# Performance work log

Measured on AMD Instinct MI355X. Metric: run time of the kernel, lower is better.

## Reference

```python
import jax, jax.numpy as jnp
import numpy as np

N_NODES = 100000
N_EDGES = 3200000
EMB_DIM = 128


def setup_inputs() -> dict:
    key = jax.random.key(0)
    k_emb, k_w1, k_w2, k_e = jax.random.split(key, 4)
    emb = jax.random.normal(k_emb, (N_NODES, EMB_DIM), dtype=jnp.float32)
    W1 = jax.random.normal(k_w1, (EMB_DIM, 64), dtype=jnp.float32) * (1.0 / np.sqrt(EMB_DIM))
    b1 = jnp.zeros((64,), dtype=jnp.float32)
    W2 = jax.random.normal(k_w2, (64, 32), dtype=jnp.float32) * (1.0 / np.sqrt(64))
    b2 = jnp.zeros((32,), dtype=jnp.float32)
    edge_index = jax.random.randint(k_e, (2, N_EDGES), 0, N_NODES, dtype=jnp.int64)
    return {"embedding": emb, "W1": W1, "b1": b1, "W2": W2, "b2": b2,
            "edge_index": edge_index}


def gcn_conv(x, W, b, src, dst, n):
    # PyG GCNConv defaults: add self-loops, symmetric normalization D^-1/2 (A+I) D^-1/2,
    # linear transform first, then gather-scale-scatter aggregation, then bias.
    xw = x @ W                                                  # [N, out]
    ones = jnp.ones(src.shape, dtype=xw.dtype)
    deg = jax.ops.segment_sum(ones, dst, num_segments=n) + 1.0  # in-degree + self-loop
    dis = jax.lax.rsqrt(deg)                                    # deg >= 1 always
    norm = dis[src] * dis[dst]                                  # [E]
    agg = jax.ops.segment_sum(xw[src] * norm[:, None], dst, num_segments=n)
    agg = agg + (dis * dis)[:, None] * xw                       # self-loop messages
    return agg + b


def reference(embedding, W1, b1, W2, b2, edge_index):
    n = embedding.shape[0]
    src, dst = edge_index[0], edge_index[1]
    # encode
    h = jax.nn.relu(gcn_conv(embedding, W1, b1, src, dst, n))
    z = gcn_conv(h, W2, b2, src, dst, n)                        # [N, 32]
    # decode: per-edge gather-dot-sigmoid
    logits = jnp.sum(z[src] * z[dst], axis=1)                   # [E]
    return jax.nn.sigmoid(logits)
```

## Files before the change

### kernel.cpp

```cpp
#include <hip/hip_runtime.h>
#include <hip/hip_bf16.h>
#include <math.h>

#define NN 100000
#define NE 3200000
#define NPAD 100096
#define NB 196
#define BN 512
#define EPB 8192
#define NBLK 391

typedef __attribute__((ext_vector_type(8))) short short8;
typedef __attribute__((ext_vector_type(4))) float floatx4;

__device__ __forceinline__ unsigned short bf16_of(float x) {
    __hip_bfloat16 h = __float2bfloat16(x);
    return *(unsigned short*)&h;
}
__device__ __forceinline__ unsigned pack2(float a, float b) {
    return (unsigned)bf16_of(a) | ((unsigned)bf16_of(b) << 16);
}
__device__ __forceinline__ float lo_f(unsigned u) { return __uint_as_float(u << 16); }
__device__ __forceinline__ float hi_f(unsigned u) { return __uint_as_float(u & 0xffff0000u); }
__device__ __forceinline__ void acc8(float* a, uint4 r) {
    a[0] += lo_f(r.x); a[1] += hi_f(r.x);
    a[2] += lo_f(r.y); a[3] += hi_f(r.y);
    a[4] += lo_f(r.z); a[5] += hi_f(r.z);
    a[6] += lo_f(r.w); a[7] += hi_f(r.w);
}

__global__ __launch_bounds__(256) void hist_kernel(const int* __restrict__ dst,
                                                   int* __restrict__ blkhist) {
    __shared__ int cnt[NB];
    int t = threadIdx.x;
    for (int i = t; i < NB; i += 256) cnt[i] = 0;
    __syncthreads();
    int e0 = blockIdx.x * EPB;
    int e1 = min(e0 + EPB, NE);
    for (int e = e0 + t; e < e1; e += 256) atomicAdd(&cnt[dst[e] >> 9], 1);
    __syncthreads();
    for (int i = t; i < NB; i += 256) blkhist[i * NBLK + blockIdx.x] = cnt[i];
}

__global__ __launch_bounds__(64) void scanA_kernel(int* __restrict__ blkhist,
                                                   int* __restrict__ totals) {
    int j = blockIdx.x, lane = threadIdx.x;
    int base = j * NBLK;
    int carry = 0;
    for (int c = 0; c < NBLK; c += 64) {
        int b = c + lane;
        int v = (b < NBLK) ? blkhist[base + b] : 0;
        int inc = v;
#pragma unroll
        for (int m = 1; m < 64; m <<= 1) {
            int u = __shfl_up(inc, m, 64);
            if (lane >= m) inc += u;
        }
        if (b < NBLK) blkhist[base + b] = carry + inc - v;
        carry += __shfl(inc, 63, 64);
    }
    if (lane == 0) totals[j] = carry;
}

__global__ __launch_bounds__(256) void scanB_kernel(const int* __restrict__ totals,
                                                    int* __restrict__ bucket_base) {
    __shared__ int sm[NB];
    int t = threadIdx.x;
    if (t < NB) sm[t] = totals[t];
    __syncthreads();
    if (t == 0) {
        int r = 0;
        for (int i = 0; i < NB; ++i) { bucket_base[i] = r; r += sm[i]; }
        bucket_base[NB] = r;
    }
}

__global__ __launch_bounds__(256) void scatter_kernel(const int* __restrict__ src,
                                                      const int* __restrict__ dst,
                                                      const int* __restrict__ blkhist,
                                                      const int* __restrict__ bucket_base,
                                                      int* __restrict__ staged) {
    __shared__ int cnt[NB];
    __shared__ int lbase[NB + 1];
    __shared__ int gbase[NB];
    __shared__ int sbuf[EPB];
    __shared__ unsigned char sbkt[EPB];
    int t = threadIdx.x;
    for (int i = t; i < NB; i += 256) cnt[i] = 0;
    __syncthreads();
    int e0 = blockIdx.x * EPB;
    int e1 = min(e0 + EPB, NE);
    int cn = e1 - e0;
    for (int e = e0 + t; e < e1; e += 256) atomicAdd(&cnt[dst[e] >> 9], 1);
    __syncthreads();
    if (t < 64) {
        int v[4]; int s = 0;
#pragma unroll
        for (int k = 0; k < 4; ++k) { int idx = t * 4 + k; v[k] = (idx < NB) ? cnt[idx] : 0; s += v[k]; }
        int inc = s;
#pragma unroll
        for (int m = 1; m < 64; m <<= 1) {
            int u = __shfl_up(inc, m, 64);
            if (t >= m) inc += u;
        }
        int run = inc - s;
#pragma unroll
        for (int k = 0; k < 4; ++k) { int idx = t * 4 + k; if (idx < NB) lbase[idx] = run; run += v[k]; }
        if (t == 63) lbase[NB] = inc;
    }
    __syncthreads();
    for (int i = t; i < NB; i += 256) {
        gbase[i] = bucket_base[i] + blkhist[i * NBLK + blockIdx.x];
        cnt[i] = lbase[i];
    }
    __syncthreads();
    for (int e = e0 + t; e < e1; e += 256) {
        int s = src[e], d = dst[e];
        int bk = d >> 9;
        int r = atomicAdd(&cnt[bk], 1);
        sbuf[r] = (s << 9) | (d & (BN - 1));
        sbkt[r] = (unsigned char)bk;
    }
    __syncthreads();
    for (int i = t; i < cn; i += 256) {
        int bk = sbkt[i];
        staged[gbase[bk] + i - lbase[bk]] = sbuf[i];
    }
}

__global__ __launch_bounds__(256) void fine_kernel(const int* __restrict__ staged,
                                                   const int* __restrict__ bucket_base,
                                                   int* __restrict__ offset,
                                                   float* __restrict__ dis,
                                                   int* __restrict__ csr_src) {
    __shared__ int hist[BN];
    __shared__ int offs[BN];
    __shared__ int cur[BN];
    int t = threadIdx.x, j = blockIdx.x;
    int bb = bucket_base[j], be = bucket_base[j + 1];
    for (int i = t; i < BN; i += 256) hist[i] = 0;
    __syncthreads();
    for (int e = bb + t; e < be; e += 256) atomicAdd(&hist[staged[e] & (BN - 1)], 1);
    __syncthreads();
    if (t < 64) {
        int v[8]; int s = 0;
#pragma unroll
        for (int k = 0; k < 8; ++k) { v[k] = hist[t * 8 + k]; s += v[k]; }
        int inc = s;
#pragma unroll
        for (int m = 1; m < 64; m <<= 1) {
            int u = __shfl_up(inc, m, 64);
            if (t >= m) inc += u;
        }
        int run = inc - s;
#pragma unroll
        for (int k = 0; k < 8; ++k) { offs[t * 8 + k] = run; run += v[k]; }
    }
    __syncthreads();
    for (int l = t; l < BN; l += 256) {
        cur[l] = offs[l];
        int n = j * BN + l;
        if (n < NN) {
            offset[n] = bb + offs[l];
            dis[n] = rsqrtf((float)hist[l] + 1.0f);
        }
    }
    if (j == NB - 1 && t == 0) offset[NN] = NE;
    __syncthreads();
    for (int e = bb + t; e < be; e += 256) {
        int p = staged[e];
        int r = atomicAdd(&cur[p & (BN - 1)], 1);
        csr_src[bb + r] = p >> 9;
    }
}

__global__ __launch_bounds__(256) void mm1_kernel(const float* __restrict__ x,
                                                  const float* __restrict__ W,
                                                  const float* __restrict__ dis,
                                                  unsigned short* __restrict__ y) {
    __shared__ unsigned short Wt[64][136];
    int t = threadIdx.x;
    for (int i = t; i < 128 * 64; i += 256) {
        int k = i >> 6, n = i & 63;
        Wt[n][k] = bf16_of(W[i]);
    }
    __syncthreads();
    int wave = t >> 6, lane = t & 63;
    int quad = lane >> 4, n16 = lane & 15;
    short8 bfr[4][4];
#pragma unroll
    for (int s = 0; s < 4; ++s)
#pragma unroll
        for (int tt = 0; tt < 4; ++tt)
            bfr[s][tt] = *(const short8*)&Wt[tt * 16 + n16][s * 32 + quad * 8];
    int tile0 = (blockIdx.x * 4 + wave) * 4;
#pragma unroll 1
    for (int it = 0; it < 4; ++it) {
        int tile = tile0 + it;
        if (tile >= 6250) break;
        int m0 = tile * 16;
        const float* xp = x + (size_t)(m0 + n16) * 128 + quad * 8;
        floatx4 acc0 = {0,0,0,0}, acc1 = {0,0,0,0}, acc2 = {0,0,0,0}, acc3 = {0,0,0,0};
#pragma unroll
        for (int s = 0; s < 4; ++s) {
            float4 lo = *(const float4*)(xp + s * 32);
            float4 hi = *(const float4*)(xp + s * 32 + 4);
            short8 a;
            a[0] = (short)bf16_of(lo.x); a[1] = (short)bf16_of(lo.y);
            a[2] = (short)bf16_of(lo.z); a[3] = (short)bf16_of(lo.w);
            a[4] = (short)bf16_of(hi.x); a[5] = (short)bf16_of(hi.y);
            a[6] = (short)bf16_of(hi.z); a[7] = (short)bf16_of(hi.w);
            acc0 = __builtin_amdgcn_mfma_f32_16x16x32_bf16(a, bfr[s][0], acc0, 0, 0, 0);
            acc1 = __builtin_amdgcn_mfma_f32_16x16x32_bf16(a, bfr[s][1], acc1, 0, 0, 0);
            acc2 = __builtin_amdgcn_mfma_f32_16x16x32_bf16(a, bfr[s][2], acc2, 0, 0, 0);
            acc3 = __builtin_amdgcn_mfma_f32_16x16x32_bf16(a, bfr[s][3], acc3, 0, 0, 0);
        }
#pragma unroll
        for (int r = 0; r < 4; ++r) {
            int ro = m0 + quad * 4 + r;
            float sc = dis[ro];
            unsigned short* yp = y + (size_t)ro * 64 + n16;
            yp[0]  = bf16_of(acc0[r] * sc);
            yp[16] = bf16_of(acc1[r] * sc);
            yp[32] = bf16_of(acc2[r] * sc);
            yp[48] = bf16_of(acc3[r] * sc);
        }
    }
}

__global__ __launch_bounds__(256) void mm2_kernel(const unsigned short* __restrict__ h,
                                                  const float* __restrict__ W,
                                                  const float* __restrict__ dis,
                                                  unsigned short* __restrict__ y) {
    __shared__ unsigned short Wt[32][72];
    int t = threadIdx.x;
    for (int i = t; i < 64 * 32; i += 256) {
        int k = i >> 5, n = i & 31;
        Wt[n][k] = bf16_of(W[i]);
    }
    __syncthreads();
    int wave = t >> 6, lane = t & 63;
    int quad = lane >> 4, n16 = lane & 15;
    short8 bfr[2][2];
#pragma unroll
    for (int s = 0; s < 2; ++s)
#pragma unroll
        for (int tt = 0; tt < 2; ++tt)
            bfr[s][tt] = *(const short8*)&Wt[tt * 16 + n16][s * 32 + quad * 8];
    int tile0 = (blockIdx.x * 4 + wave) * 4;
#pragma unroll 1
    for (int it = 0; it < 4; ++it) {
        int tile = tile0 + it;
        if (tile >= 6250) break;
        int m0 = tile * 16;
        const unsigned short* hp = h + (size_t)(m0 + n16) * 64 + quad * 8;
        floatx4 acc0 = {0,0,0,0}, acc1 = {0,0,0,0};
#pragma unroll
        for (int s = 0; s < 2; ++s) {
            short8 a = *(const short8*)(hp + s * 32);
            acc0 = __builtin_amdgcn_mfma_f32_16x16x32_bf16(a, bfr[s][0], acc0, 0, 0, 0);
            acc1 = __builtin_amdgcn_mfma_f32_16x16x32_bf16(a, bfr[s][1], acc1, 0, 0, 0);
        }
#pragma unroll
        for (int r = 0; r < 4; ++r) {
            int ro = m0 + quad * 4 + r;
            float sc = dis[ro];
            unsigned short* yp = y + (size_t)ro * 32 + n16;
            yp[0]  = bf16_of(acc0[r] * sc);
            yp[16] = bf16_of(acc1[r] * sc);
        }
    }
}

__global__ __launch_bounds__(256) void agg64_kernel(const uint4* __restrict__ ys4,
                                                    const float* __restrict__ dis,
                                                    const int* __restrict__ offset,
                                                    const int* __restrict__ csr_src,
                                                    const float* __restrict__ b,
                                                    uint4* __restrict__ h4) {
    int tid = blockIdx.x * 256 + threadIdx.x;
    int nd = tid >> 3, c = tid & 7;
    if (nd >= NN) return;
    int start = offset[nd], end = offset[nd + 1];
    float acc[8] = {0, 0, 0, 0, 0, 0, 0, 0};
    acc8(acc, ys4[(size_t)nd * 8 + c]);
    int i = start;
    int n8 = start + ((end - start) & ~7);
    for (; i < n8; i += 8) {
        int s0 = csr_src[i],     s1 = csr_src[i + 1], s2 = csr_src[i + 2], s3 = csr_src[i + 3];
        int s4 = csr_src[i + 4], s5 = csr_src[i + 5], s6 = csr_src[i + 6], s7 = csr_src[i + 7];
        uint4 r0 = ys4[(size_t)s0 * 8 + c];
        uint4 r1 = ys4[(size_t)s1 * 8 + c];
        uint4 r2 = ys4[(size_t)s2 * 8 + c];
        uint4 r3 = ys4[(size_t)s3 * 8 + c];
        uint4 r4 = ys4[(size_t)s4 * 8 + c];
        uint4 r5 = ys4[(size_t)s5 * 8 + c];
        uint4 r6 = ys4[(size_t)s6 * 8 + c];
        uint4 r7 = ys4[(size_t)s7 * 8 + c];
        acc8(acc, r0); acc8(acc, r1); acc8(acc, r2); acc8(acc, r3);
        acc8(acc, r4); acc8(acc, r5); acc8(acc, r6); acc8(acc, r7);
    }
    for (; i < end; ++i) acc8(acc, ys4[(size_t)csr_src[i] * 8 + c]);
    float ds = dis[nd];
    const float4 bv0 = *(const float4*)&b[c * 8];
    const float4 bv1 = *(const float4*)&b[c * 8 + 4];
    uint4 o;
    o.x = pack2(fmaxf(fmaf(ds, acc[0], bv0.x), 0.f), fmaxf(fmaf(ds, acc[1], bv0.y), 0.f));
    o.y = pack2(fmaxf(fmaf(ds, acc[2], bv0.z), 0.f), fmaxf(fmaf(ds, acc[3], bv0.w), 0.f));
    o.z = pack2(fmaxf(fmaf(ds, acc[4], bv1.x), 0.f), fmaxf(fmaf(ds, acc[5], bv1.y), 0.f));
    o.w = pack2(fmaxf(fmaf(ds, acc[6], bv1.z), 0.f), fmaxf(fmaf(ds, acc[7], bv1.w), 0.f));
    h4[(size_t)nd * 8 + c] = o;
}

__global__ __launch_bounds__(256) void agg32_kernel(const uint4* __restrict__ ys4,
                                                    const float* __restrict__ dis,
                                                    const int* __restrict__ offset,
                                                    const int* __restrict__ csr_src,
                                                    const float* __restrict__ b,
                                                    uint4* __restrict__ z4) {
    int tid = blockIdx.x * 256 + threadIdx.x;
    int nd = tid >> 2, c = tid & 3;
    if (nd >= NN) return;
    int start = offset[nd], end = offset[nd + 1];
    float acc[8] = {0, 0, 0, 0, 0, 0, 0, 0};
    acc8(acc, ys4[(size_t)nd * 4 + c]);
    int i = start;
    int n8 = start + ((end - start) & ~7);
    for (; i < n8; i += 8) {
        int s0 = csr_src[i],     s1 = csr_src[i + 1], s2 = csr_src[i + 2], s3 = csr_src[i + 3];
        int s4 = csr_src[i + 4], s5 = csr_src[i + 5], s6 = csr_src[i + 6], s7 = csr_src[i + 7];
        uint4 r0 = ys4[(size_t)s0 * 4 + c];
        uint4 r1 = ys4[(size_t)s1 * 4 + c];
        uint4 r2 = ys4[(size_t)s2 * 4 + c];
        uint4 r3 = ys4[(size_t)s3 * 4 + c];
        uint4 r4 = ys4[(size_t)s4 * 4 + c];
        uint4 r5 = ys4[(size_t)s5 * 4 + c];
        uint4 r6 = ys4[(size_t)s6 * 4 + c];
        uint4 r7 = ys4[(size_t)s7 * 4 + c];
        acc8(acc, r0); acc8(acc, r1); acc8(acc, r2); acc8(acc, r3);
        acc8(acc, r4); acc8(acc, r5); acc8(acc, r6); acc8(acc, r7);
    }
    for (; i < end; ++i) acc8(acc, ys4[(size_t)csr_src[i] * 4 + c]);
    float ds = dis[nd];
    const float4 bv0 = *(const float4*)&b[c * 8];
    const float4 bv1 = *(const float4*)&b[c * 8 + 4];
    uint4 o;
    o.x = pack2(fmaf(ds, acc[0], bv0.x), fmaf(ds, acc[1], bv0.y));
    o.y = pack2(fmaf(ds, acc[2], bv0.z), fmaf(ds, acc[3], bv0.w));
    o.z = pack2(fmaf(ds, acc[4], bv1.x), fmaf(ds, acc[5], bv1.y));
    o.w = pack2(fmaf(ds, acc[6], bv1.z), fmaf(ds, acc[7], bv1.w));
    z4[(size_t)nd * 4 + c] = o;
}

__global__ __launch_bounds__(256) void decode_kernel(const uint4* __restrict__ z4,
                                                     const int* __restrict__ src,
                                                     const int* __restrict__ dst,
                                                     float* __restrict__ out) {
    int tid = blockIdx.x * 256 + threadIdx.x;
    int e = tid >> 2, k = tid & 3;
    if (e >= NE) return;
    int s = src[e], d = dst[e];
    uint4 ra = z4[(size_t)s * 4 + k];
    uint4 rb = z4[(size_t)d * 4 + k];
    float acc;
    acc  = lo_f(ra.x) * lo_f(rb.x) + hi_f(ra.x) * hi_f(rb.x);
    acc += lo_f(ra.y) * lo_f(rb.y) + hi_f(ra.y) * hi_f(rb.y);
    acc += lo_f(ra.z) * lo_f(rb.z) + hi_f(ra.z) * hi_f(rb.z);
    acc += lo_f(ra.w) * lo_f(rb.w) + hi_f(ra.w) * hi_f(rb.w);
#pragma unroll
    for (int m = 2; m >= 1; m >>= 1) acc += __shfl_xor(acc, m, 4);
    if (k == 0) out[e] = 1.0f / (1.0f + expf(-acc));
}

extern "C" void kernel_launch(void* const* d_in, const int* in_sizes, int n_in,
                              void* d_out, int out_size, void* d_ws, size_t ws_size,
                              hipStream_t stream) {
    const float* emb = (const float*)d_in[0];
    const float* W1  = (const float*)d_in[1];
    const float* b1  = (const float*)d_in[2];
    const float* W2  = (const float*)d_in[3];
    const float* b2  = (const float*)d_in[4];
    const int*   ei  = (const int*)d_in[5];
    const int* src = ei;
    const int* dst = ei + NE;
    float* out = (float*)d_out;

    char* w = (char*)d_ws;
    int*   offset      = (int*)w;           w += (size_t)NPAD * 4;
    float* dis         = (float*)w;         w += (size_t)NPAD * 4;
    int*   bucket_base = (int*)w;           w += 1024;
    int*   totals      = (int*)w;           w += 1024;
    int*   blkhist     = (int*)w;           w += 307200;
    int*   csr_src     = (int*)w;           w += (size_t)NE * 4;
    int*   staged      = (int*)w;           w += (size_t)NE * 4;
    unsigned short* ysbuf = (unsigned short*)w; w += (size_t)NN * 64 * 2;
    unsigned short* h  = (unsigned short*)w;
    unsigned short* ys1 = ysbuf;
    unsigned short* ys2 = ysbuf;
    unsigned short* z   = ysbuf + (size_t)NN * 32;

    hist_kernel<<<NBLK, 256, 0, stream>>>(dst, blkhist);
    scanA_kernel<<<NB, 64, 0, stream>>>(blkhist, totals);
    scanB_kernel<<<1, 256, 0, stream>>>(totals, bucket_base);
    scatter_kernel<<<NBLK, 256, 0, stream>>>(src, dst, blkhist, bucket_base, staged);
    fine_kernel<<<NB, 256, 0, stream>>>(staged, bucket_base, offset, dis, csr_src);

    mm1_kernel<<<391, 256, 0, stream>>>(emb, W1, dis, ys1);
    agg64_kernel<<<(NN * 8) / 256, 256, 0, stream>>>((const uint4*)ys1, dis, offset, csr_src, b1, (uint4*)h);

    mm2_kernel<<<391, 256, 0, stream>>>(h, W2, dis, ys2);
    agg32_kernel<<<(NN * 4 + 255) / 256, 256, 0, stream>>>((const uint4*)ys2, dis, offset, csr_src, b2, (uint4*)z);

    decode_kernel<<<(NE * 4) / 256, 256, 0, stream>>>((const uint4*)z, src, dst, out);
}
```

Baseline: 363.3 us.

## Fuse layer-1 aggregation with second matmul and use fp16 dot2 in decode

The layer-1 aggregation now keeps each 32-node tile of ReLU'd hidden rows in shared memory and runs the 64x32 MFMA matmul in the same kernel. This removes the global write and re-read of the hidden matrix and one kernel launch. Separately, z is stored as fp16 instead of bf16 so the decode kernel can use the packed fdot2 instruction for the per-edge dot product. The scatter bucket-tag array widens to 16-bit, and workspace buffers are laid out separately. Costs: only half the waves do the fused matmul, the block has an extra barrier, and fp16 has narrower range than bf16.

```diff
diff --git a/kernel.cpp b/kernel.cpp
--- a/kernel.cpp
+++ b/kernel.cpp
@@ -12,6 +12,7 @@
 
 typedef __attribute__((ext_vector_type(8))) short short8;
 typedef __attribute__((ext_vector_type(4))) float floatx4;
+typedef _Float16 h2_t __attribute__((ext_vector_type(2)));
 
 __device__ __forceinline__ unsigned short bf16_of(float x) {
     __hip_bfloat16 h = __float2bfloat16(x);
@@ -27,6 +28,21 @@
     a[2] += lo_f(r.y); a[3] += hi_f(r.y);
     a[4] += lo_f(r.z); a[5] += hi_f(r.z);
     a[6] += lo_f(r.w); a[7] += hi_f(r.w);
+}
+
+__device__ __forceinline__ unsigned packh2(float a, float b) {
+    unsigned short ua = __builtin_bit_cast(unsigned short, (_Float16)a);
+    unsigned short ub = __builtin_bit_cast(unsigned short, (_Float16)b);
+    return (unsigned)ua | ((unsigned)ub << 16);
+}
+__device__ __forceinline__ float dot2acc(unsigned a, unsigned b, float acc) {
+#if __has_builtin(__builtin_amdgcn_fdot2)
+    return __builtin_amdgcn_fdot2(__builtin_bit_cast(h2_t, a),
+                                  __builtin_bit_cast(h2_t, b), acc, false);
+#else
+    h2_t ha = __builtin_bit_cast(h2_t, a), hb = __builtin_bit_cast(h2_t, b);
+    return acc + (float)ha[0] * (float)hb[0] + (float)ha[1] * (float)hb[1];
+#endif
 }
 
 __global__ __launch_bounds__(256) void hist_kernel(const int* __restrict__ dst,
@@ -84,7 +100,7 @@
     __shared__ int lbase[NB + 1];
     __shared__ int gbase[NB];
     __shared__ int sbuf[EPB];
-    __shared__ unsigned char sbkt[EPB];
+    __shared__ unsigned short sbkt[EPB];
     int t = threadIdx.x;
     for (int i = t; i < NB; i += 256) cnt[i] = 0;
     __syncthreads();
@@ -119,7 +135,7 @@
         int bk = d >> 9;
         int r = atomicAdd(&cnt[bk], 1);
         sbuf[r] = (s << 9) | (d & (BN - 1));
-        sbkt[r] = (unsigned char)bk;
+        sbkt[r] = (unsigned short)bk;
     }
     __syncthreads();
     for (int i = t; i < cn; i += 256) {
@@ -228,59 +244,21 @@
     }
 }
 
-__global__ __launch_bounds__(256) void mm2_kernel(const unsigned short* __restrict__ h,
-                                                  const float* __restrict__ W,
-                                                  const float* __restrict__ dis,
-                                                  unsigned short* __restrict__ y) {
+__global__ __launch_bounds__(256) void agg64mm2_kernel(
+    const uint4* __restrict__ ys4, const float* __restrict__ dis,
+    const int* __restrict__ offset, const int* __restrict__ csr_src,
+    const float* __restrict__ b1, const float* __restrict__ W2,
+    unsigned short* __restrict__ y2)
+{
+    __shared__ unsigned hrow[32][36];
     __shared__ unsigned short Wt[32][72];
     int t = threadIdx.x;
     for (int i = t; i < 64 * 32; i += 256) {
         int k = i >> 5, n = i & 31;
-        Wt[n][k] = bf16_of(W[i]);
-    }
-    __syncthreads();
-    int wave = t >> 6, lane = t & 63;
-    int quad = lane >> 4, n16 = lane & 15;
-    short8 bfr[2][2];
-#pragma unroll
-    for (int s = 0; s < 2; ++s)
-#pragma unroll
-        for (int tt = 0; tt < 2; ++tt)
-            bfr[s][tt] = *(const short8*)&Wt[tt * 16 + n16][s * 32 + quad * 8];
-    int tile0 = (blockIdx.x * 4 + wave) * 4;
-#pragma unroll 1
-    for (int it = 0; it < 4; ++it) {
-        int tile = tile0 + it;
-        if (tile >= 6250) break;
-        int m0 = tile * 16;
-        const unsigned short* hp = h + (size_t)(m0 + n16) * 64 + quad * 8;
-        floatx4 acc0 = {0,0,0,0}, acc1 = {0,0,0,0};
-#pragma unroll
-        for (int s = 0; s < 2; ++s) {
-            short8 a = *(const short8*)(hp + s * 32);
-            acc0 = __builtin_amdgcn_mfma_f32_16x16x32_bf16(a, bfr[s][0], acc0, 0, 0, 0);
-            acc1 = __builtin_amdgcn_mfma_f32_16x16x32_bf16(a, bfr[s][1], acc1, 0, 0, 0);
-        }
-#pragma unroll
-        for (int r = 0; r < 4; ++r) {
-            int ro = m0 + quad * 4 + r;
-            float sc = dis[ro];
-            unsigned short* yp = y + (size_t)ro * 32 + n16;
-            yp[0]  = bf16_of(acc0[r] * sc);
-            yp[16] = bf16_of(acc1[r] * sc);
-        }
-    }
-}
-
-__global__ __launch_bounds__(256) void agg64_kernel(const uint4* __restrict__ ys4,
-                                                    const float* __restrict__ dis,
-                                                    const int* __restrict__ offset,
-                                                    const int* __restrict__ csr_src,
-                                                    const float* __restrict__ b,
-                                                    uint4* __restrict__ h4) {
-    int tid = blockIdx.x * 256 + threadIdx.x;
-    int nd = tid >> 3, c = tid & 7;
-    if (nd >= NN) return;
+        Wt[n][k] = bf16_of(W2[i]);
+    }
+    int n0 = blockIdx.x * 32;
+    int nd = n0 + (t >> 3), c = t & 7;
     int start = offset[nd], end = offset[nd + 1];
     float acc[8] = {0, 0, 0, 0, 0, 0, 0, 0};
     acc8(acc, ys4[(size_t)nd * 8 + c]);
@@ -301,15 +279,38 @@
         acc8(acc, r4); acc8(acc, r5); acc8(acc, r6); acc8(acc, r7);
     }
     for (; i < end; ++i) acc8(acc, ys4[(size_t)csr_src[i] * 8 + c]);
-    float ds = dis[nd];
-    const float4 bv0 = *(const float4*)&b[c * 8];
-    const float4 bv1 = *(const float4*)&b[c * 8 + 4];
-    uint4 o;
-    o.x = pack2(fmaxf(fmaf(ds, acc[0], bv0.x), 0.f), fmaxf(fmaf(ds, acc[1], bv0.y), 0.f));
-    o.y = pack2(fmaxf(fmaf(ds, acc[2], bv0.z), 0.f), fmaxf(fmaf(ds, acc[3], bv0.w), 0.f));
-    o.z = pack2(fmaxf(fmaf(ds, acc[4], bv1.x), 0.f), fmaxf(fmaf(ds, acc[5], bv1.y), 0.f));
-    o.w = pack2(fmaxf(fmaf(ds, acc[6], bv1.z), 0.f), fmaxf(fmaf(ds, acc[7], bv1.w), 0.f));
-    h4[(size_t)nd * 8 + c] = o;
+    {
+        float ds = dis[nd];
+        const float4 bv0 = *(const float4*)&b1[c * 8];
+        const float4 bv1 = *(const float4*)&b1[c * 8 + 4];
+        uint4 o;
+        o.x = pack2(fmaxf(fmaf(ds, acc[0], bv0.x), 0.f), fmaxf(fmaf(ds, acc[1], bv0.y), 0.f));
+        o.y = pack2(fmaxf(fmaf(ds, acc[2], bv0.z), 0.f), fmaxf(fmaf(ds, acc[3], bv0.w), 0.f));
+        o.z = pack2(fmaxf(fmaf(ds, acc[4], bv1.x), 0.f), fmaxf(fmaf(ds, acc[5], bv1.y), 0.f));
+        o.w = pack2(fmaxf(fmaf(ds, acc[6], bv1.z), 0.f), fmaxf(fmaf(ds, acc[7], bv1.w), 0.f));
+        *(uint4*)&hrow[t >> 3][c * 4] = o;
+    }
+    __syncthreads();
+    if (t < 128) {
+        int w = t >> 6, lane = t & 63;
+        int quad = lane >> 4, n16 = lane & 15;
+        floatx4 acc0 = {0, 0, 0, 0}, acc1 = {0, 0, 0, 0};
+#pragma unroll
+        for (int s = 0; s < 2; ++s) {
+            short8 a = *(const short8*)((const char*)&hrow[w * 16 + n16][0] + s * 64 + quad * 16);
+            short8 bf0 = *(const short8*)&Wt[n16][s * 32 + quad * 8];
+            short8 bf1 = *(const short8*)&Wt[16 + n16][s * 32 + quad * 8];
+            acc0 = __builtin_amdgcn_mfma_f32_16x16x32_bf16(a, bf0, acc0, 0, 0, 0);
+            acc1 = __builtin_amdgcn_mfma_f32_16x16x32_bf16(a, bf1, acc1, 0, 0, 0);
+        }
+#pragma unroll
+        for (int r = 0; r < 4; ++r) {
+            int ro = n0 + w * 16 + quad * 4 + r;
+            float sc = dis[ro];
+            y2[(size_t)ro * 32 + n16]      = bf16_of(acc0[r] * sc);
+            y2[(size_t)ro * 32 + 16 + n16] = bf16_of(acc1[r] * sc);
+        }
+    }
 }
 
 __global__ __launch_bounds__(256) void agg32_kernel(const uint4* __restrict__ ys4,
@@ -345,10 +346,10 @@
     const float4 bv0 = *(const float4*)&b[c * 8];
     const float4 bv1 = *(const float4*)&b[c * 8 + 4];
     uint4 o;
-    o.x = pack2(fmaf(ds, acc[0], bv0.x), fmaf(ds, acc[1], bv0.y));
-    o.y = pack2(fmaf(ds, acc[2], bv0.z), fmaf(ds, acc[3], bv0.w));
-    o.z = pack2(fmaf(ds, acc[4], bv1.x), fmaf(ds, acc[5], bv1.y));
-    o.w = pack2(fmaf(ds, acc[6], bv1.z), fmaf(ds, acc[7], bv1.w));
+    o.x = packh2(fmaf(ds, acc[0], bv0.x), fmaf(ds, acc[1], bv0.y));
+    o.y = packh2(fmaf(ds, acc[2], bv0.z), fmaf(ds, acc[3], bv0.w));
+    o.z = packh2(fmaf(ds, acc[4], bv1.x), fmaf(ds, acc[5], bv1.y));
+    o.w = packh2(fmaf(ds, acc[6], bv1.z), fmaf(ds, acc[7], bv1.w));
     z4[(size_t)nd * 4 + c] = o;
 }
 
@@ -362,13 +363,12 @@
     int s = src[e], d = dst[e];
     uint4 ra = z4[(size_t)s * 4 + k];
     uint4 rb = z4[(size_t)d * 4 + k];
-    float acc;
-    acc  = lo_f(ra.x) * lo_f(rb.x) + hi_f(ra.x) * hi_f(rb.x);
-    acc += lo_f(ra.y) * lo_f(rb.y) + hi_f(ra.y) * hi_f(rb.y);
-    acc += lo_f(ra.z) * lo_f(rb.z) + hi_f(ra.z) * hi_f(rb.z);
-    acc += lo_f(ra.w) * lo_f(rb.w) + hi_f(ra.w) * hi_f(rb.w);
-#pragma unroll
-    for (int m = 2; m >= 1; m >>= 1) acc += __shfl_xor(acc, m, 4);
+    float acc = dot2acc(ra.x, rb.x, 0.f);
+    acc = dot2acc(ra.y, rb.y, acc);
+    acc = dot2acc(ra.z, rb.z, acc);
+    acc = dot2acc(ra.w, rb.w, acc);
+    acc += __shfl_xor(acc, 1, 4);
+    acc += __shfl_xor(acc, 2, 4);
     if (k == 0) out[e] = 1.0f / (1.0f + expf(-acc));
 }
 
@@ -390,14 +390,12 @@
     float* dis         = (float*)w;         w += (size_t)NPAD * 4;
     int*   bucket_base = (int*)w;           w += 1024;
     int*   totals      = (int*)w;           w += 1024;
-    int*   blkhist     = (int*)w;           w += 307200;
+    int*   blkhist     = (int*)w;           w += (size_t)NB * NBLK * 4 + 1024;
     int*   csr_src     = (int*)w;           w += (size_t)NE * 4;
     int*   staged      = (int*)w;           w += (size_t)NE * 4;
-    unsigned short* ysbuf = (unsigned short*)w; w += (size_t)NN * 64 * 2;
-    unsigned short* h  = (unsigned short*)w;
-    unsigned short* ys1 = ysbuf;
-    unsigned short* ys2 = ysbuf;
-    unsigned short* z   = ysbuf + (size_t)NN * 32;
+    unsigned short* ys1 = (unsigned short*)w; w += (size_t)NN * 64 * 2;
+    unsigned short* ys2 = (unsigned short*)w; w += (size_t)NN * 32 * 2;
+    unsigned short* z   = (unsigned short*)w; w += (size_t)NN * 32 * 2;
 
     hist_kernel<<<NBLK, 256, 0, stream>>>(dst, blkhist);
     scanA_kernel<<<NB, 64, 0, stream>>>(blkhist, totals);
@@ -406,10 +404,9 @@
     fine_kernel<<<NB, 256, 0, stream>>>(staged, bucket_base, offset, dis, csr_src);
 
     mm1_kernel<<<391, 256, 0, stream>>>(emb, W1, dis, ys1);
-    agg64_kernel<<<(NN * 8) / 256, 256, 0, stream>>>((const uint4*)ys1, dis, offset, csr_src, b1, (uint4*)h);
-
-    mm2_kernel<<<391, 256, 0, stream>>>(h, W2, dis, ys2);
-    agg32_kernel<<<(NN * 4 + 255) / 256, 256, 0, stream>>>((const uint4*)ys2, dis, offset, csr_src, b2, (uint4*)z);
-
+    agg64mm2_kernel<<<NN / 32, 256, 0, stream>>>((const uint4*)ys1, dis, offset, csr_src,
+                                                 b1, W2, ys2);
+    agg32_kernel<<<(NN * 4 + 255) / 256, 256, 0, stream>>>((const uint4*)ys2, dis, offset,
+                                                           csr_src, b2, (uint4*)z);
     decode_kernel<<<(NE * 4) / 256, 256, 0, stream>>>((const uint4*)z, src, dst, out);
 }
```

After: 421.3 us. 1.16x slower.
